# Kernel optimization log

Hardware: AMD Instinct MI355X
Metric: run time of the kernel (lower is better)

Reference implementation:

```python
import jax, jax.numpy as jnp
import numpy as np

# Faithful JAX reference for MVLiftingModule.lift_2D_to_3D with lifting_method='mean'.
# Torch semantics: for each batch, view, and part p in [1, parts_nb[b]] (in order),
# scatter-write the (weighted softmax) pixel prediction into each point that any
# Since each pixel's predicted part is unique (argmax), the winning pixel per point
# is the one maximizing key = pred_class * H*W + flat_pixel_index. We compute that
# deterministically via scatter-max, then gather features and voint-mean over views.

def setup_inputs() -> dict:
    key = jax.random.key(0)
    k1, k2, k3, k4, k5 = jax.random.split(key, 5)
    B, N, V, C, H, W = 4, 2048, 12, 50, 128, 128
    points = jax.random.normal(k1, (B, N, 3), dtype=jnp.float32)
    predictions_2d = jax.random.normal(k2, (B, V, C, H, W), dtype=jnp.float32)
    # -1 marks background pixels (no point), as in pytorch3d pix_to_face
    rendered_pix_to_point = jax.random.randint(k3, (B, V, 1, H, W), -1, N, dtype=jnp.int32)
    views_weights = jax.random.uniform(k4, (B, V, 1, 1, 1), dtype=jnp.float32)
    parts_nb = jax.random.randint(k5, (B,), 1, 7, dtype=jnp.int32)
    return {"points": points, "predictions_2d": predictions_2d,
            "rendered_pix_to_point": rendered_pix_to_point,
            "views_weights": views_weights, "parts_nb": parts_nb}


def reference(points, predictions_2d, rendered_pix_to_point, views_weights, parts_nb):
    B, N, _ = points.shape
    _, V, C, H, W = predictions_2d.shape
    P = H * W

    p2p = rendered_pix_to_point[:, :, 0]            # (B,V,H,W)
    valid = p2p != -1                                # pix_to_face_mask
    idx = jnp.where(valid, p2p % N, 0)               # invalid pixels -> point 0 (as in torch)

    probs = jax.nn.softmax(predictions_2d, axis=2)   # softmax over classes
    pred_max = jnp.argmax(probs, axis=2).astype(jnp.int32)   # (B,V,H,W)
    feats = (views_weights * probs).reshape(B, V, C, P)       # weighted predictions

    # pixel participates iff valid and its predicted part in [1, parts_nb[b]]
    mask_pix = valid & (pred_max >= 1) & (pred_max <= parts_nb[:, None, None, None])
    mask_pix = mask_pix.reshape(B, V, P)
    idx_f = idx.reshape(B, V, P)

    pix = jnp.arange(P, dtype=jnp.int32)
    kkey = pred_max.reshape(B, V, P) * P + pix
    kkey = jnp.where(mask_pix, kkey, -1)

    bi = jnp.arange(B)[:, None, None]
    vi = jnp.arange(V)[None, :, None]
    winner = jnp.full((B, V, N), -1, dtype=jnp.int32).at[bi, vi, idx_f].max(kkey)

    voints_mask = (winner >= 0)                      # (B,V,N)
    win_pix = jnp.where(voints_mask, winner % P, 0)  # winning pixel per point/view

    # gather weighted features at winning pixel: (B,V,C,N)
    point_feats = jnp.take_along_axis(feats, win_pix[:, :, None, :], axis=3)
    m = voints_mask.astype(feats.dtype)
    masked = point_feats * m[:, :, None, :]

    # vointmean: masked mean over views -> (B,C,N)
    denom = jnp.maximum(m.sum(axis=1), 1.0)          # (B,N)
    labels_3d_feats = masked.sum(axis=1) / denom[:, None, :]
    return labels_3d_feats
```

## Files before the change

kernel.cpp:

```cpp
#include <hip/hip_runtime.h>

#define B 4
#define N 2048
#define V 12
#define C 50
#define P 16384
#define CP 64

__global__ __launch_bounds__(256) void k1_argmax_scatter(
    const float4* __restrict__ predv,
    const int4*  __restrict__ p2pv,
    const int*   __restrict__ parts_nb,
    int*         __restrict__ winner) {
  const int PQ = P / 4;
  int t = blockIdx.x * 256 + threadIdx.x;
  if (t >= B * V * PQ) return;
  int q  = t % PQ;
  int bv = t / PQ;
  int b  = bv / V;

  size_t base = (size_t)bv * C * PQ + q;
  float4 x = predv[base];
  float m0 = x.x, m1 = x.y, m2 = x.z, m3 = x.w;
  int   a0 = 0,  a1 = 0,  a2 = 0,  a3 = 0;
  for (int c = 1; c < C; ++c) {
    float4 y = predv[base + (size_t)c * PQ];
    if (y.x > m0) { m0 = y.x; a0 = c; }
    if (y.y > m1) { m1 = y.y; a1 = c; }
    if (y.z > m2) { m2 = y.z; a2 = c; }
    if (y.w > m3) { m3 = y.w; a3 = c; }
  }

  int4 pt = p2pv[(size_t)bv * PQ + q];
  int pn = parts_nb[b];
  int p0 = q * 4;
  int* wbase = winner + bv * N;
  if (pt.x != -1 && a0 >= 1 && a0 <= pn) atomicMax(wbase + pt.x, a0 * P + p0);
  if (pt.y != -1 && a1 >= 1 && a1 <= pn) atomicMax(wbase + pt.y, a1 * P + p0 + 1);
  if (pt.z != -1 && a2 >= 1 && a2 <= pn) atomicMax(wbase + pt.z, a2 * P + p0 + 2);
  if (pt.w != -1 && a3 >= 1 && a3 <= pn) atomicMax(wbase + pt.w, a3 * P + p0 + 3);
}

__global__ __launch_bounds__(256) void k1b_extract(
    const float* __restrict__ pred,
    const int*   __restrict__ p2p,
    const int*   __restrict__ winner,
    const float* __restrict__ vw,
    float*       __restrict__ wfeat) {
  int t = blockIdx.x * 256 + threadIdx.x;
  int p  = t & (P - 1);
  int bv = t >> 14;

  int pt = p2p[(size_t)bv * P + p];
  if (pt == -1) return;
  int bvn = bv * N + pt;
  int key = winner[bvn];
  if (key < 0 || (key & (P - 1)) != p) return;

  const float* pp = pred + (size_t)bv * C * P + p;
  float e[C];
  float s = 0.f;
  #pragma unroll
  for (int c = 0; c < C; ++c) e[c] = pp[(size_t)c * P];
  #pragma unroll
  for (int c = 0; c < C; ++c) { e[c] = __expf(e[c]); s += e[c]; }
  float w = vw[bv] / s;

  float4* dst = (float4*)(wfeat + (size_t)bvn * CP);
  #pragma unroll
  for (int c4 = 0; c4 < C / 4; ++c4) {
    dst[c4] = make_float4(e[4*c4] * w, e[4*c4+1] * w, e[4*c4+2] * w, e[4*c4+3] * w);
  }
  wfeat[(size_t)bvn * CP + 48] = e[48] * w;
  wfeat[(size_t)bvn * CP + 49] = e[49] * w;
}

__global__ __launch_bounds__(256) void k3_reduce(
    const int*   __restrict__ winner,
    const float* __restrict__ wfeat,
    float*       __restrict__ out) {
  int wid  = blockIdx.x * 4 + (threadIdx.x >> 6);
  int lane = threadIdx.x & 63;
  int b = wid >> 11;
  int n = wid & (N - 1);

  float acc = 0.f;
  int cnt = 0;
  #pragma unroll
  for (int v = 0; v < V; ++v) {
    int bvn = (b * V + v) * N + n;
    bool valid = winner[bvn] >= 0;
    float f = (valid && lane < C) ? wfeat[(size_t)bvn * CP + lane] : 0.f;
    cnt += valid ? 1 : 0;
    acc += f;
  }
  if (lane < C)
    out[((size_t)b * C + lane) * N + n] = acc / (float)(cnt > 0 ? cnt : 1);
}

extern "C" void kernel_launch(void* const* d_in, const int* in_sizes, int n_in,
                              void* d_out, int out_size, void* d_ws, size_t ws_size,
                              hipStream_t stream) {
  const float* pred  = (const float*)d_in[1];
  const int*   p2p   = (const int*)d_in[2];
  const float* vw    = (const float*)d_in[3];
  const int*   parts = (const int*)d_in[4];
  float* out = (float*)d_out;

  int*   winner = (int*)d_ws;
  float* wfeat  = (float*)((char*)d_ws + (size_t)B * V * N * sizeof(int));

  hipMemsetAsync(winner, 0xFF, (size_t)B * V * N * sizeof(int), stream);

  int nthreads1 = B * V * (P / 4);
  k1_argmax_scatter<<<(nthreads1 + 255) / 256, 256, 0, stream>>>(
      (const float4*)pred, (const int4*)p2p, parts, winner);

  int nthreads1b = B * V * P;
  k1b_extract<<<nthreads1b / 256, 256, 0, stream>>>(
      pred, p2p, winner, vw, wfeat);

  k3_reduce<<<(B * N) / 4, 256, 0, stream>>>(winner, wfeat, out);
}
```

Before: 259.8 us.

## Vectorize extract kernel over four pixels and defer softmax normalization to reduce

The extract kernel now has each thread handle four consecutive pixels using float4 loads across all classes, instead of one scalar pixel per thread. This gives coalesced 16-byte reads of the prediction tensor. Winning pixels write unnormalized exponentials as scalar per-class stores, and the row sum goes to a separate buffer. The reduce kernel applies view weight divided by sum, which avoids a per-thread register array. The cost is that every pixel thread now streams all 50 classes even when none of its four pixels won, and the scattered scalar stores are less efficient than the old float4 stores.

```diff
diff --git a/kernel.cpp b/kernel.cpp
--- a/kernel.cpp
+++ b/kernel.cpp
@@ -41,43 +41,55 @@
   if (pt.w != -1 && a3 >= 1 && a3 <= pn) atomicMax(wbase + pt.w, a3 * P + p0 + 3);
 }
 
-__global__ __launch_bounds__(256) void k1b_extract(
-    const float* __restrict__ pred,
-    const int*   __restrict__ p2p,
+__global__ __launch_bounds__(256) void k2_extract(
+    const float4* __restrict__ predv,
+    const int4*  __restrict__ p2pv,
     const int*   __restrict__ winner,
-    const float* __restrict__ vw,
-    float*       __restrict__ wfeat) {
+    float*       __restrict__ wfeat,
+    float*       __restrict__ wsum) {
+  const int PQ = P / 4;
   int t = blockIdx.x * 256 + threadIdx.x;
-  int p  = t & (P - 1);
-  int bv = t >> 14;
+  if (t >= B * V * PQ) return;
+  int q  = t % PQ;
+  int bv = t / PQ;
 
-  int pt = p2p[(size_t)bv * P + p];
-  if (pt == -1) return;
-  int bvn = bv * N + pt;
-  int key = winner[bvn];
-  if (key < 0 || (key & (P - 1)) != p) return;
+  int4 pt = p2pv[(size_t)bv * PQ + q];
+  int p0 = q * 4;
+  const int* wb = winner + bv * N;
 
-  const float* pp = pred + (size_t)bv * C * P + p;
-  float e[C];
-  float s = 0.f;
-  #pragma unroll
-  for (int c = 0; c < C; ++c) e[c] = pp[(size_t)c * P];
-  #pragma unroll
-  for (int c = 0; c < C; ++c) { e[c] = __expf(e[c]); s += e[c]; }
-  float w = vw[bv] / s;
+  bool w0 = false, w1 = false, w2 = false, w3 = false;
+  int n0 = 0, n1 = 0, n2 = 0, n3 = 0;
+  if (pt.x != -1) { int k = wb[pt.x]; w0 = (k >= 0) && ((k & (P-1)) == p0    ); n0 = bv * N + pt.x; }
+  if (pt.y != -1) { int k = wb[pt.y]; w1 = (k >= 0) && ((k & (P-1)) == p0 + 1); n1 = bv * N + pt.y; }
+  if (pt.z != -1) { int k = wb[pt.z]; w2 = (k >= 0) && ((k & (P-1)) == p0 + 2); n2 = bv * N + pt.z; }
+  if (pt.w != -1) { int k = wb[pt.w]; w3 = (k >= 0) && ((k & (P-1)) == p0 + 3); n3 = bv * N + pt.w; }
 
-  float4* dst = (float4*)(wfeat + (size_t)bvn * CP);
-  #pragma unroll
-  for (int c4 = 0; c4 < C / 4; ++c4) {
-    dst[c4] = make_float4(e[4*c4] * w, e[4*c4+1] * w, e[4*c4+2] * w, e[4*c4+3] * w);
+  float* d0 = wfeat + (size_t)n0 * CP;
+  float* d1 = wfeat + (size_t)n1 * CP;
+  float* d2 = wfeat + (size_t)n2 * CP;
+  float* d3 = wfeat + (size_t)n3 * CP;
+
+  size_t base = (size_t)bv * C * PQ + q;
+  float s0 = 0.f, s1 = 0.f, s2 = 0.f, s3 = 0.f;
+  for (int c = 0; c < C; ++c) {
+    float4 y = predv[base + (size_t)c * PQ];
+    float e0 = __expf(y.x), e1 = __expf(y.y), e2 = __expf(y.z), e3 = __expf(y.w);
+    if (w0) { d0[c] = e0; s0 += e0; }
+    if (w1) { d1[c] = e1; s1 += e1; }
+    if (w2) { d2[c] = e2; s2 += e2; }
+    if (w3) { d3[c] = e3; s3 += e3; }
   }
-  wfeat[(size_t)bvn * CP + 48] = e[48] * w;
-  wfeat[(size_t)bvn * CP + 49] = e[49] * w;
+  if (w0) wsum[n0] = s0;
+  if (w1) wsum[n1] = s1;
+  if (w2) wsum[n2] = s2;
+  if (w3) wsum[n3] = s3;
 }
 
 __global__ __launch_bounds__(256) void k3_reduce(
     const int*   __restrict__ winner,
     const float* __restrict__ wfeat,
+    const float* __restrict__ wsum,
+    const float* __restrict__ vw,
     float*       __restrict__ out) {
   int wid  = blockIdx.x * 4 + (threadIdx.x >> 6);
   int lane = threadIdx.x & 63;
@@ -90,9 +102,10 @@
   for (int v = 0; v < V; ++v) {
     int bvn = (b * V + v) * N + n;
     bool valid = winner[bvn] >= 0;
-    float f = (valid && lane < C) ? wfeat[(size_t)bvn * CP + lane] : 0.f;
+    float e = (valid && lane < C) ? wfeat[(size_t)bvn * CP + lane] : 0.f;
+    float f = valid ? (vw[b * V + v] / wsum[bvn]) : 0.f;
     cnt += valid ? 1 : 0;
-    acc += f;
+    acc += e * f;
   }
   if (lane < C)
     out[((size_t)b * C + lane) * N + n] = acc / (float)(cnt > 0 ? cnt : 1);
@@ -107,18 +120,19 @@
   const int*   parts = (const int*)d_in[4];
   float* out = (float*)d_out;
 
-  int*   winner = (int*)d_ws;
-  float* wfeat  = (float*)((char*)d_ws + (size_t)B * V * N * sizeof(int));
+  char* ws = (char*)d_ws;
+  int*   winner = (int*)ws;                         ws += (size_t)B * V * N * sizeof(int);
+  float* wsum   = (float*)ws;                       ws += (size_t)B * V * N * sizeof(float);
+  float* wfeat  = (float*)ws;
 
   hipMemsetAsync(winner, 0xFF, (size_t)B * V * N * sizeof(int), stream);
 
-  int nthreads1 = B * V * (P / 4);
-  k1_argmax_scatter<<<(nthreads1 + 255) / 256, 256, 0, stream>>>(
+  int nthreads = B * V * (P / 4);
+  k1_argmax_scatter<<<(nthreads + 255) / 256, 256, 0, stream>>>(
       (const float4*)pred, (const int4*)p2p, parts, winner);
 
-  int nthreads1b = B * V * P;
-  k1b_extract<<<nthreads1b / 256, 256, 0, stream>>>(
-      pred, p2p, winner, vw, wfeat);
+  k2_extract<<<(nthreads + 255) / 256, 256, 0, stream>>>(
+      (const float4*)pred, (const int4*)p2p, winner, wfeat, wsum);
 
-  k3_reduce<<<(B * N) / 4, 256, 0, stream>>>(winner, wfeat, out);
+  k3_reduce<<<(B * N) / 4, 256, 0, stream>>>(winner, wfeat, wsum, vw, out);
 }
```

Result: slower. 293.5 us (+13.0%).
